# Kernel optimization log

Measured on AMD Instinct MI355X. Metric: run time of the kernel, lower is better.

Reference implementation:

```python
import jax, jax.numpy as jnp
import numpy as np

B, C, K, F = 16, 64, 128, 6
HORIZON_S = 3.0  # conflict_horizon_s default
EPS = 1e-06


def setup_inputs() -> dict:
    rng = np.random.default_rng(0)
    # base adjacency: sparse random directed graph, zero diagonal
    A = (rng.random((B, K, K)) < 0.05).astype(np.float32)
    A[:, np.arange(K), np.arange(K)] = 0.0
    # candidates: exactly one unordered-pair edit (state in {0:none,1:i->j,2:j->i})
    cand = np.repeat(A[:, None], C, axis=1).copy()
    i = rng.integers(0, K - 1, (B, C))
    j = i + 1 + (rng.integers(0, K - 1, (B, C)) % (K - 1 - i))
    state = rng.integers(0, 3, (B, C))
    bidx = np.arange(B)[:, None] * np.ones((1, C), dtype=np.int64)
    cidx = np.ones((B, 1), dtype=np.int64) * np.arange(C)[None, :]
    cand[bidx, cidx, i, j] = (state == 1).astype(np.float32)
    cand[bidx, cidx, j, i] = (state == 2).astype(np.float32)
    cand[:, 0] = A  # candidate 0 is NOOP (keep A_t)
    # agent features: (x, y, yaw, vx, vy, pad)
    feat = rng.normal(size=(B, K, F)).astype(np.float32)
    feat[..., 0:2] *= 20.0  # spread positions over ~40m
    mask = (rng.random((B, K)) > 0.1).astype(np.float32)
    return {
        "A_t": jnp.asarray(A),
        "candidate_A": jnp.asarray(cand),
        "agent_feat": jnp.asarray(feat),
        "agent_mask": jnp.asarray(mask),
    }


def _edit_tokens(A_t, candidate_A):
    # vectorized version of EBSTM.extract_edit_tokens
    Bn, Cn, Kn, _ = candidate_A.shape
    base = A_t > 0.5                      # [B,K,K]
    cb = candidate_A > 0.5                # [B,C,K,K]
    diff = cb != base[:, None]            # [B,C,K,K]
    upper = jnp.triu(jnp.ones((Kn, Kn), dtype=bool), k=1)
    pairdiff = (diff | jnp.swapaxes(diff, -1, -2)) & upper
    flat = pairdiff.reshape(Bn, Cn, Kn * Kn)
    changed = flat.any(-1)                # [B,C]
    idx = jnp.argmax(flat, axis=-1)       # first changed pair in row-major (i,j) order
    i = idx // Kn
    j = idx % Kn
    barange = jnp.arange(Bn)[:, None]
    carange = jnp.arange(Cn)[None, :]
    b_ij = base[barange, i, j]
    b_ji = base[barange, j, i]
    c_ij = cb[barange, carange, i, j]
    c_ji = cb[barange, carange, j, i]
    prev = jnp.where(b_ij & ~b_ji, 1, jnp.where(b_ji & ~b_ij, 2, 0))
    nxt = jnp.where(c_ij & ~c_ji, 1, jnp.where(c_ji & ~c_ij, 2, 0))
    tokens = jnp.stack([i, j, prev, nxt], axis=-1).astype(jnp.int32)
    return tokens * changed[..., None].astype(jnp.int32)


def _relation_state3(cb):
    # cb: bool [B,C,K,K]
    at = jnp.swapaxes(cb, -1, -2)
    return ((cb & ~at).astype(jnp.int32) * 1
            + (~cb & at).astype(jnp.int32) * 2
            + (cb & at).astype(jnp.int32) * 3)


def _batched_acyclic(cb, agent_mask):
    # vectorized Kahn zero-indegree peel, matching EBSTM._is_acyclic semantics:
    #  - indegree counts edges from ALL sources (valid or not)
    #  - only valid nodes are ever removed
    #  - special case: <=1 valid node is acyclic
    Bn, Cn, Kn, _ = cb.shape
    valid = (agent_mask > 0.5)[:, None, :]           # [B,1,K]
    Ai = cb.astype(jnp.int32)                        # [B,C,K,K]
    indeg = Ai.sum(axis=-2) * valid.astype(jnp.int32)  # [B,C,K]
    removed = jnp.zeros((Bn, Cn, Kn), dtype=bool)

    def body(t, carry):
        indeg, removed = carry
        rem = valid & (~removed) & (indeg == 0)
        dec = jnp.einsum('bci,bcij->bcj', rem.astype(jnp.int32), Ai)
        return indeg - dec, removed | rem

    indeg, removed = jax.lax.fori_loop(0, Kn, body, (indeg, removed))
    vcount = valid.astype(jnp.int32).sum(-1)          # [B,1]
    return (removed.astype(jnp.int32).sum(-1) == vcount) | (vcount <= 1)


def _pair_dists(agent_feat):
    pos = agent_feat[..., 0:2]
    vel = agent_feat[..., 3:5]
    # _pair_distance: d[b,i,j] = |pos_i - pos_j|
    d = jnp.linalg.norm(pos[:, :, None] - pos[:, None, :], axis=-1)
    # _pair_closest_approach_distance: r[b,i,j] = pos_j - pos_i
    r = pos[:, None, :] - pos[:, :, None]
    v = vel[:, None, :] - vel[:, :, None]
    vv = (v * v).sum(-1)
    rv = (r * v).sum(-1)
    t_star = jnp.clip(-rv / (vv + EPS), 0.0, HORIZON_S)
    dmin = jnp.linalg.norm(r + v * t_star[..., None], axis=-1)
    eye = jnp.eye(dmin.shape[-1], dtype=bool)[None]
    dmin = jnp.where(eye, jnp.inf, dmin)
    return jnp.stack([d, dmin], axis=0)  # [2,B,K,K]


def reference(A_t, candidate_A, agent_feat, agent_mask):
    cb = candidate_A > 0.5
    tokens = _edit_tokens(A_t, candidate_A)          # [B,C,4] int32
    rel = _relation_state3(cb)                       # [B,C,K,K] int32
    acyclic = _batched_acyclic(cb, agent_mask)       # [B,C] bool
    dists = _pair_dists(agent_feat)                  # [2,B,K,K] float32
    return tokens, rel, acyclic, dists
```

## Files before the change

### kernel.cpp

```cpp
#include <hip/hip_runtime.h>
#include <cstdint>
#include <math.h>

#define KN 128
#define BATCH 16
#define CAND 64

typedef float vfloat4 __attribute__((ext_vector_type(4)));

static constexpr size_t TOK_OFF = 0;
static constexpr size_t REL_OFF = (size_t)BATCH * CAND * 4;
static constexpr size_t ACY_OFF = REL_OFF + (size_t)BATCH * CAND * KN * KN;
static constexpr size_t DST_OFF = ACY_OFF + (size_t)BATCH * CAND;

#define DIAG_BIG 1.0e30f

__global__ __launch_bounds__(256) void prep_kernel(const float* __restrict__ A_t,
                                                   const float* __restrict__ feat,
                                                   uint32_t* __restrict__ bits,
                                                   float* __restrict__ out) {
    int t = threadIdx.x;
    {
        int tid  = blockIdx.x * 256 + t;
        int wave = tid >> 6;
        int lane = tid & 63;
        int half = wave & 1;
        int row  = wave >> 1;
        float v = A_t[(size_t)row * KN + half * 64 + lane];
        unsigned long long m = __ballot(v > 0.5f);
        if (lane == 0) {
            bits[row * 4 + half * 2]     = (uint32_t)m;
            bits[row * 4 + half * 2 + 1] = (uint32_t)(m >> 32);
        }
    }
    {
        int bi = 2 * blockIdx.x + (t >> 7);
        int b2 = bi >> 7, i = bi & 127, j = t & 127;
        const float* fi = feat + (size_t)bi * 6;
        const float* fj = feat + (size_t)(b2 * KN + j) * 6;
        float pix = fi[0], piy = fi[1], vix = fi[3], viy = fi[4];
        float pjx = fj[0], pjy = fj[1], vjx = fj[3], vjy = fj[4];
        float dx = pix - pjx, dy = piy - pjy;
        float d = sqrtf(dx * dx + dy * dy);
        float rx = pjx - pix, ry = pjy - piy;
        float vx = vjx - vix, vy = vjy - viy;
        float vv = vx * vx + vy * vy;
        float rv = rx * vx + ry * vy;
        float ts = fminf(fmaxf(-rv / (vv + 1e-6f), 0.0f), 3.0f);
        float mx = rx + vx * ts, my = ry + vy * ts;
        float dmin = (i == j) ? DIAG_BIG : sqrtf(mx * mx + my * my);
        float* o = out + DST_OFF;
        __builtin_nontemporal_store(d,    o + (size_t)(b2 * KN + i) * KN + j);
        __builtin_nontemporal_store(dmin, o + (size_t)((BATCH + b2) * KN + i) * KN + j);
    }
}

__global__ __launch_bounds__(256) void main_kernel(const float* __restrict__ cand,
                                                   const float* __restrict__ mask,
                                                   const uint32_t* __restrict__ baseBits,
                                                   float* __restrict__ out) {
    __shared__ uint32_t adj[KN][5];
    __shared__ uint32_t adjT[KN][6];
    __shared__ uint32_t baseB[KN][4];
    __shared__ int storeChunk;

    const int t    = threadIdx.x;
    const int lane = t & 63;
    const int wave = t >> 6;
    const int bc   = blockIdx.x;
    const int b    = bc >> 6;

    const float* cptr = cand + (size_t)bc * (KN * KN);
    float* relp = out + REL_OFF + (size_t)bc * (KN * KN);

    float4 c[16];
    const int sub = lane & 31;
    #pragma unroll
    for (int m = 0; m < 16; ++m) {
        int r = (m * 4 + wave) * 2 + (lane >> 5);
        c[m] = ((const float4*)(cptr + (size_t)r * KN))[sub];
    }

    if (t == 0) storeChunk = 0;

    if (wave == 0) {
        #pragma unroll
        for (int s = 0; s < 8; ++s) {
            int w = lane + 64 * s;
            baseB[w >> 2][w & 3] = baseBits[b * 512 + w];
        }
    }

    #pragma unroll
    for (int m = 0; m < 16; ++m) {
        int r = (m * 4 + wave) * 2 + (lane >> 5);
        const float4 v = c[m];
        uint32_t nib = (v.x > 0.5f ? 1u : 0u) | (v.y > 0.5f ? 2u : 0u) |
                       (v.z > 0.5f ? 4u : 0u) | (v.w > 0.5f ? 8u : 0u);
        uint32_t word = nib << (4 * (sub & 7));
        word |= __shfl_xor(word, 1);
        word |= __shfl_xor(word, 2);
        word |= __shfl_xor(word, 4);
        if ((lane & 7) == 0) adj[r][sub >> 3] = word;
    }
    __syncthreads();

    {
        const int h = wave >> 1, q = wave & 1;
        uint32_t rw0 = adj[h * 64 + lane][q * 2];
        uint32_t rw1 = adj[h * 64 + lane][q * 2 + 1];
        uint32_t myLo = 0, myHi = 0;
        #pragma unroll
        for (int cc = 0; cc < 64; ++cc) {
            uint32_t w = (cc < 32) ? rw0 : rw1;
            unsigned long long m = __ballot((w >> (cc & 31)) & 1u);
            if (lane == cc) { myLo = (uint32_t)m; myHi = (uint32_t)(m >> 32); }
        }
        adjT[q * 64 + lane][2 * h]     = myLo;
        adjT[q * 64 + lane][2 * h + 1] = myHi;
    }
    __syncthreads();

    if (wave == 0) {
        unsigned long long v1 = __ballot(mask[b * KN + lane]      > 0.5f);
        unsigned long long v2 = __ballot(mask[b * KN + 64 + lane] > 0.5f);

        int cmin = 0x7fffffff;
        #pragma unroll
        for (int s = 0; s < 8; ++s) {
            int idx = lane + 64 * s;
            int i = idx >> 2, k = idx & 3;
            uint32_t diff = adj[i][k] ^ baseB[i][k];
            if (diff) {
                int base = k * 32;
                uint32_t up, low;
                if (i < base)            { up = diff; low = 0u; }
                else if (i >= base + 31) { up = 0u; low = (i > base + 31) ? diff : (diff & 0x7fffffffu); }
                else {
                    int sft = i - base;
                    up  = diff & (0xffffffffu << (sft + 1));
                    low = diff & ((1u << sft) - 1u);
                }
                int c1 = 0x7fffffff, c2 = 0x7fffffff;
                if (up)  c1 = (i << 7) | (base + __builtin_ctz(up));
                if (low) { int cc2 = base + __builtin_ctz(low); c2 = (cc2 << 7) | i; }
                cmin = min(cmin, min(c1, c2));
            }
        }
        #pragma unroll
        for (int off = 32; off > 0; off >>= 1) cmin = min(cmin, __shfl_down(cmin, off));

        if (lane == 0) {
            float* tok = out + TOK_OFF + (size_t)bc * 4;
            if (cmin != 0x7fffffff) {
                int i = cmin >> 7, j = cmin & 127;
                uint32_t b_ij = (baseB[i][j >> 5] >> (j & 31)) & 1u;
                uint32_t b_ji = (baseB[j][i >> 5] >> (i & 31)) & 1u;
                uint32_t c_ij = (adj[i][j >> 5] >> (j & 31)) & 1u;
                uint32_t c_ji = (adj[j][i >> 5] >> (i & 31)) & 1u;
                int prev = (b_ij && !b_ji) ? 1 : ((b_ji && !b_ij) ? 2 : 0);
                int nxt  = (c_ij && !c_ji) ? 1 : ((c_ji && !c_ij) ? 2 : 0);
                tok[0] = (float)i; tok[1] = (float)j; tok[2] = (float)prev; tok[3] = (float)nxt;
            } else {
                tok[0] = 0.f; tok[1] = 0.f; tok[2] = 0.f; tok[3] = 0.f;
            }
        }

        uint32_t a0 = adjT[lane][0],      a1 = adjT[lane][1];
        uint32_t a2 = adjT[lane][2],      a3 = adjT[lane][3];
        uint32_t d0 = adjT[lane + 64][0], d1 = adjT[lane + 64][1];
        uint32_t d2 = adjT[lane + 64][2], d3 = adjT[lane + 64][3];
        const bool val1 = (v1 >> lane) & 1ull;
        const bool val2 = (v2 >> lane) & 1ull;
        int id1 = val1 ? (__popc(a0) + __popc(a1) + __popc(a2) + __popc(a3)) : 0;
        int id2 = val2 ? (__popc(d0) + __popc(d1) + __popc(d2) + __popc(d3)) : 0;
        bool rm1 = false, rm2 = false;
        for (int it = 0; it < KN; ++it) {
            bool r1 = val1 && !rm1 && (id1 == 0);
            bool r2 = val2 && !rm2 && (id2 == 0);
            unsigned long long m1 = __ballot(r1);
            unsigned long long m2 = __ballot(r2);
            if ((m1 | m2) == 0ull) break;
            rm1 = rm1 || r1;
            rm2 = rm2 || r2;
            uint32_t r0w = (uint32_t)m1, r1w = (uint32_t)(m1 >> 32);
            uint32_t r2w = (uint32_t)m2, r3w = (uint32_t)(m2 >> 32);
            id1 -= __popc(r0w & a0) + __popc(r1w & a1) + __popc(r2w & a2) + __popc(r3w & a3);
            id2 -= __popc(r0w & d0) + __popc(r1w & d1) + __popc(r2w & d2) + __popc(r3w & d3);
        }
        unsigned long long rmm1 = __ballot(rm1);
        unsigned long long rmm2 = __ballot(rm2);
        if (lane == 0) {
            int rc = __popcll(rmm1) + __popcll(rmm2);
            int vc = __popcll(v1) + __popcll(v2);
            out[ACY_OFF + bc] = ((rc == vc) || (vc <= 1)) ? 1.0f : 0.0f;
        }
    }

    for (;;) {
        int ch = 0;
        if (lane == 0) ch = atomicAdd(&storeChunk, 1);
        ch = __shfl(ch, 0);
        if (ch >= 16) break;
        #pragma unroll
        for (int ii = 0; ii < 4; ++ii) {
            int q  = ch * 256 + ii * 64 + lane;
            int i  = q >> 5;
            int j0 = (q & 31) * 4;
            int iw = j0 >> 5, sh = j0 & 31;
            uint32_t wij = adj[i][iw];
            uint32_t wti = adjT[i][iw];
            vfloat4 o;
            o.x = (float)(((wij >> (sh + 0)) & 1u) + 2u * ((wti >> (sh + 0)) & 1u));
            o.y = (float)(((wij >> (sh + 1)) & 1u) + 2u * ((wti >> (sh + 1)) & 1u));
            o.z = (float)(((wij >> (sh + 2)) & 1u) + 2u * ((wti >> (sh + 2)) & 1u));
            o.w = (float)(((wij >> (sh + 3)) & 1u) + 2u * ((wti >> (sh + 3)) & 1u));
            __builtin_nontemporal_store(o, ((vfloat4*)relp) + q);
        }
    }
}

extern "C" void kernel_launch(void* const* d_in, const int* in_sizes, int n_in,
                              void* d_out, int out_size, void* d_ws, size_t ws_size,
                              hipStream_t stream) {
    const float* A_t  = (const float*)d_in[0];
    const float* cand = (const float*)d_in[1];
    const float* feat = (const float*)d_in[2];
    const float* mask = (const float*)d_in[3];
    float* out = (float*)d_out;
    uint32_t* bits = (uint32_t*)d_ws;

    prep_kernel<<<1024, 256, 0, stream>>>(A_t, feat, bits, out);
    main_kernel<<<BATCH * CAND, 256, 0, stream>>>(cand, mask, bits, out);
}
```

Before: 126.0 us.

## Fuse prep kernel into main kernel and recompute base bitmask per block

```diff
diff --git a/kernel.cpp b/kernel.cpp
--- a/kernel.cpp
+++ b/kernel.cpp
@@ -15,31 +15,44 @@
 
 #define DIAG_BIG 1.0e30f
 
-__global__ __launch_bounds__(256) void prep_kernel(const float* __restrict__ A_t,
-                                                   const float* __restrict__ feat,
-                                                   uint32_t* __restrict__ bits,
-                                                   float* __restrict__ out) {
-    int t = threadIdx.x;
+__global__ __launch_bounds__(256) void fused_kernel(const float* __restrict__ A_t,
+                                                    const float* __restrict__ cand,
+                                                    const float* __restrict__ feat,
+                                                    const float* __restrict__ mask,
+                                                    float* __restrict__ out) {
+    __shared__ uint32_t adj[KN][5];
+    __shared__ uint32_t adjT[KN][6];
+    __shared__ uint32_t baseB[KN][4];
+    __shared__ int storeChunk;
+
+    const int t    = threadIdx.x;
+    const int lane = t & 63;
+    const int wave = t >> 6;
+    const int bc   = blockIdx.x;
+    const int b    = bc >> 6;
+
+    const float* cptr = cand + (size_t)bc * (KN * KN);
+    const float* aptr = A_t  + (size_t)b  * (KN * KN);
+    float* relp = out + REL_OFF + (size_t)bc * (KN * KN);
+
+    const int bi = 2 * bc + (t >> 7);
+    const int b2 = bi >> 7, di = bi & 127, dj = t & 127;
+    const float* fi = feat + (size_t)bi * 6;
+    const float* fj = feat + (size_t)(b2 * KN + dj) * 6;
+    float pix = fi[0], piy = fi[1], vix = fi[3], viy = fi[4];
+    float pjx = fj[0], pjy = fj[1], vjx = fj[3], vjy = fj[4];
+
+    float4 c[16];
+    const int sub = lane & 31;
+    #pragma unroll
+    for (int m = 0; m < 16; ++m) {
+        int r = (m * 4 + wave) * 2 + (lane >> 5);
+        c[m] = ((const float4*)(cptr + (size_t)r * KN))[sub];
+    }
+
+    if (t == 0) storeChunk = 0;
+
     {
-        int tid  = blockIdx.x * 256 + t;
-        int wave = tid >> 6;
-        int lane = tid & 63;
-        int half = wave & 1;
-        int row  = wave >> 1;
-        float v = A_t[(size_t)row * KN + half * 64 + lane];
-        unsigned long long m = __ballot(v > 0.5f);
-        if (lane == 0) {
-            bits[row * 4 + half * 2]     = (uint32_t)m;
-            bits[row * 4 + half * 2 + 1] = (uint32_t)(m >> 32);
-        }
-    }
-    {
-        int bi = 2 * blockIdx.x + (t >> 7);
-        int b2 = bi >> 7, i = bi & 127, j = t & 127;
-        const float* fi = feat + (size_t)bi * 6;
-        const float* fj = feat + (size_t)(b2 * KN + j) * 6;
-        float pix = fi[0], piy = fi[1], vix = fi[3], viy = fi[4];
-        float pjx = fj[0], pjy = fj[1], vjx = fj[3], vjy = fj[4];
         float dx = pix - pjx, dy = piy - pjy;
         float d = sqrtf(dx * dx + dy * dy);
         float rx = pjx - pix, ry = pjy - piy;
@@ -48,47 +61,10 @@
         float rv = rx * vx + ry * vy;
         float ts = fminf(fmaxf(-rv / (vv + 1e-6f), 0.0f), 3.0f);
         float mx = rx + vx * ts, my = ry + vy * ts;
-        float dmin = (i == j) ? DIAG_BIG : sqrtf(mx * mx + my * my);
+        float dmin = (di == dj) ? DIAG_BIG : sqrtf(mx * mx + my * my);
         float* o = out + DST_OFF;
-        __builtin_nontemporal_store(d,    o + (size_t)(b2 * KN + i) * KN + j);
-        __builtin_nontemporal_store(dmin, o + (size_t)((BATCH + b2) * KN + i) * KN + j);
-    }
-}
-
-__global__ __launch_bounds__(256) void main_kernel(const float* __restrict__ cand,
-                                                   const float* __restrict__ mask,
-                                                   const uint32_t* __restrict__ baseBits,
-                                                   float* __restrict__ out) {
-    __shared__ uint32_t adj[KN][5];
-    __shared__ uint32_t adjT[KN][6];
-    __shared__ uint32_t baseB[KN][4];
-    __shared__ int storeChunk;
-
-    const int t    = threadIdx.x;
-    const int lane = t & 63;
-    const int wave = t >> 6;
-    const int bc   = blockIdx.x;
-    const int b    = bc >> 6;
-
-    const float* cptr = cand + (size_t)bc * (KN * KN);
-    float* relp = out + REL_OFF + (size_t)bc * (KN * KN);
-
-    float4 c[16];
-    const int sub = lane & 31;
-    #pragma unroll
-    for (int m = 0; m < 16; ++m) {
-        int r = (m * 4 + wave) * 2 + (lane >> 5);
-        c[m] = ((const float4*)(cptr + (size_t)r * KN))[sub];
-    }
-
-    if (t == 0) storeChunk = 0;
-
-    if (wave == 0) {
-        #pragma unroll
-        for (int s = 0; s < 8; ++s) {
-            int w = lane + 64 * s;
-            baseB[w >> 2][w & 3] = baseBits[b * 512 + w];
-        }
+        __builtin_nontemporal_store(d,    o + (size_t)(b2 * KN + di) * KN + dj);
+        __builtin_nontemporal_store(dmin, o + (size_t)((BATCH + b2) * KN + di) * KN + dj);
     }
 
     #pragma unroll
@@ -103,6 +79,14 @@
         word |= __shfl_xor(word, 4);
         if ((lane & 7) == 0) adj[r][sub >> 3] = word;
     }
+
+    float4 a[16];
+    #pragma unroll
+    for (int m = 0; m < 16; ++m) {
+        int r = (m * 4 + wave) * 2 + (lane >> 5);
+        a[m] = ((const float4*)(aptr + (size_t)r * KN))[sub];
+    }
+
     __syncthreads();
 
     {
@@ -119,6 +103,20 @@
         adjT[q * 64 + lane][2 * h]     = myLo;
         adjT[q * 64 + lane][2 * h + 1] = myHi;
     }
+
+    #pragma unroll
+    for (int m = 0; m < 16; ++m) {
+        int r = (m * 4 + wave) * 2 + (lane >> 5);
+        const float4 v = a[m];
+        uint32_t nib = (v.x > 0.5f ? 1u : 0u) | (v.y > 0.5f ? 2u : 0u) |
+                       (v.z > 0.5f ? 4u : 0u) | (v.w > 0.5f ? 8u : 0u);
+        uint32_t word = nib << (4 * (sub & 7));
+        word |= __shfl_xor(word, 1);
+        word |= __shfl_xor(word, 2);
+        word |= __shfl_xor(word, 4);
+        if ((lane & 7) == 0) baseB[r][sub >> 3] = word;
+    }
+
     __syncthreads();
 
     if (wave == 0) {
@@ -210,11 +208,15 @@
             int iw = j0 >> 5, sh = j0 & 31;
             uint32_t wij = adj[i][iw];
             uint32_t wti = adjT[i][iw];
+            uint32_t a4 = (wij >> sh) & 0xFu;
+            uint32_t b4 = (wti >> sh) & 0xFu;
+            uint32_t packed = ((a4 * 0x00204081u) & 0x01010101u)
+                            | (((b4 * 0x00204081u) & 0x01010101u) << 1);
             vfloat4 o;
-            o.x = (float)(((wij >> (sh + 0)) & 1u) + 2u * ((wti >> (sh + 0)) & 1u));
-            o.y = (float)(((wij >> (sh + 1)) & 1u) + 2u * ((wti >> (sh + 1)) & 1u));
-            o.z = (float)(((wij >> (sh + 2)) & 1u) + 2u * ((wti >> (sh + 2)) & 1u));
-            o.w = (float)(((wij >> (sh + 3)) & 1u) + 2u * ((wti >> (sh + 3)) & 1u));
+            o.x = (float)(uint8_t)(packed);
+            o.y = (float)(uint8_t)(packed >> 8);
+            o.z = (float)(uint8_t)(packed >> 16);
+            o.w = (float)(uint8_t)(packed >> 24);
             __builtin_nontemporal_store(o, ((vfloat4*)relp) + q);
         }
     }
@@ -228,8 +230,7 @@
     const float* feat = (const float*)d_in[2];
     const float* mask = (const float*)d_in[3];
     float* out = (float*)d_out;
-    uint32_t* bits = (uint32_t*)d_ws;
-
-    prep_kernel<<<1024, 256, 0, stream>>>(A_t, feat, bits, out);
-    main_kernel<<<BATCH * CAND, 256, 0, stream>>>(cand, mask, bits, out);
+    (void)d_ws; (void)ws_size;
+
+    fused_kernel<<<BATCH * CAND, 256, 0, stream>>>(A_t, cand, feat, mask, out);
 }
```

Result: no change. 126.8 us (+0.6%).
